# Optimization experiments

Measured on AMD Instinct MI355X. Metric: run time of the kernel, lower is better.

## Reference

```python
import jax, jax.numpy as jnp
import numpy as np
from jax import lax


def _sobel_kernels3d(n1=1, n2=2, n3=2):
    Sx = np.asarray([[[-n1, 0, n1], [-n2, 0, n2], [-n1, 0, n1]],
                     [[-n2, 0, n2], [-n3 * n2, 0, n3 * n2], [-n2, 0, n2]],
                     [[-n1, 0, n1], [-n2, 0, n2], [-n1, 0, n1]]])
    Sy = np.asarray([[[-n1, -n2, -n1], [0, 0, 0], [n1, n2, n1]],
                     [[-n2, -n3 * n2, -n2], [0, 0, 0], [n2, n3 * n2, n2]],
                     [[-n1, -n2, -n1], [0, 0, 0], [n1, n2, n1]]])
    Sz = np.asarray([[[-n1, -n2, -n1], [-n2, -n3 * n2, -n2], [-n1, -n2, -n1]],
                     [[0, 0, 0], [0, 0, 0], [0, 0, 0]],
                     [[n1, n2, n1], [n2, n3 * n2, n2], [n1, n2, n1]]])
    Sd11 = np.asarray([[[0, n1, n2], [-n1, 0, n1], [-n2, -n1, 0]],
                       [[0, n2, n2 * n3], [-n2, 0, n2], [-n2 * n3, -n2, 0]],
                       [[0, n1, n2], [-n1, 0, n1], [-n2, -n1, 0]]])
    Sd12 = np.asarray([[[-n2, -n1, 0], [-n1, 0, n1], [0, n1, n2]],
                       [[-n2 * n3, -n2, 0], [-n2, 0, n2], [0, n2, n2 * n3]],
                       [[-n2, -n1, 0], [-n1, 0, n1], [0, n1, n2]]])
    Sd21 = Sd11.T
    Sd22 = Sd12.T
    Sd31 = np.asarray([-S.T for S in Sd11.T])
    Sd32 = np.asarray([S.T for S in Sd12.T])
    S = [Sx, Sy, Sz, Sd11, Sd12, Sd21, Sd22, Sd31, Sd32]
    # (9, 1, 3, 3, 3) OIDHW conv weight bank
    return np.stack(S).astype(np.float32)[:, None]


def _grad_edge3d(img, kernels, a=1):
    # img: (B, C, H, W, D); kernels: (9, 1, 3, 3, 3)
    B, C, H, W, D = img.shape
    p = jnp.pad(img, ((0, 0), (0, 0), (a, a), (a, a), (a, a)), mode='reflect')
    Hp, Wp, Dp = H + 2 * a, W + 2 * a, D + 2 * a
    # Each channel convolved independently with all 9 kernels in one conv call.
    xin = p.reshape(B * C, 1, Hp, Wp, Dp)
    conv = lax.conv_general_dilated(
        xin, kernels, window_strides=(1, 1, 1), padding='SAME',
        dimension_numbers=('NCDHW', 'OIDHW', 'NCDHW'))  # (B*C, 9, Hp, Wp, Dp)
    conv = conv.reshape(B, C, 9, Hp, Wp, Dp)
    # torch: sum_c (conv + 1e-6), squared per-filter, then sum_s (. + 1e-6), sqrt, * 1/C
    per_filter = jnp.sum(conv + 1e-6, axis=1)           # (B, 9, Hp, Wp, Dp)
    mag = jnp.sqrt(jnp.sum(per_filter ** 2, axis=1) + 9 * 1e-6) / C  # (B, Hp, Wp, Dp)
    mag = mag[:, a:-a, a:-a, a:-a]                      # (B, H, W, D)
    mn = mag.min()
    mx = mag.max()
    norm = (mag - mn) / (mx - mn + 1e-6)
    return norm.reshape(B, 1, H, W, D)


def setup_inputs() -> dict:
    key = jax.random.key(0)
    kx, ky = jax.random.split(key)
    B, C, H, W, D = 4, 1, 128, 128, 128
    x = jax.random.normal(kx, (B, C, H, W, D), dtype=jnp.float32)
    y = jax.random.normal(ky, (B, C, H, W, D), dtype=jnp.float32)
    kernels = jnp.asarray(_sobel_kernels3d(1, 2, 2))
    return {"x": x, "y": y, "kernels": kernels}


def reference(x, y, kernels):
    edge_x = _grad_edge3d(x, kernels)
    edge_y = _grad_edge3d(y, kernels)
    # lam_errors = [(1.0, L1Loss())], reduction='sum' -> 1e-6 + 1.0 * mean|ex-ey|
    l1 = jnp.mean(jnp.abs(edge_x - edge_y))
    return 1e-6 + 1.0 * l1
```

## Files before the change

### kernel.cpp

```cpp
#include <hip/hip_runtime.h>
#include <hip/hip_fp16.h>

#define HH 128
#define NB 4
#define NVOX (NB * HH * HH * HH)

#define NBLK1 1024
#define GRID2 512
#define TPB 256

typedef float vf2 __attribute__((ext_vector_type(2)));

__device__ __align__(16) unsigned int g_bmin[NBLK1];
__device__ __align__(16) unsigned int g_bmax[NBLK1];

union U4H8 { uint4 u; __half2 h[4]; };

__global__ __launch_bounds__(256) void pass1_kernel(
    const float* __restrict__ x, const float* __restrict__ y,
    __half* __restrict__ magx, __half* __restrict__ magy,
    float* __restrict__ out) {
    int bid = blockIdx.x;
    int tid = threadIdx.x;
    if (bid == 0 && tid == 0) out[0] = 0.0f;

    int lane = tid & 63, wid = tid >> 6;
    int wg  = bid & 15;
    int hs  = (bid >> 4) & 7;
    int b   = (bid >> 7) & 3;
    int img = bid >> 9;

    const float* __restrict__ src = img ? y : x;
    __half* __restrict__ dst = img ? magy : magx;

    int w0 = wg * 8 + wid * 2;
    int w1 = w0 + 1;
    int cw0 = (w0 == 0) ? 1 : (w0 - 1);
    int cw3 = (w1 == 127) ? 126 : (w1 + 1);
    int h0 = hs << 4;
    const vf2* base2 = (const vf2*)(src + ((size_t)b << 21));

    const vf2 two = {2.0f, 2.0f};
    const vf2 e1v = {1e-6f, 1e-6f};

    vf2 sbD[2][3], ubD[2][3], dbS[2][3], sbS[2][3], ubS[2][3], dbU[2][3], sbU[2][3];
    float mn = 3.4e38f, mx = 0.0f;
    bool l0 = (lane == 0), l63 = (lane == 63);

    auto cstage = [&](vf2 q, vf2& S, vf2& D, vf2& U) {
        float Lxs = __shfl_up(q.y, 1);
        float Rys = __shfl_down(q.x, 1);
        float Lx = l0  ? q.y : Lxs;
        float Ry = l63 ? q.x : Rys;
        vf2 LV = {Lx, q.x};
        vf2 RV = {q.y, Ry};
        vf2 t = LV + RV;
        S = __builtin_elementwise_fma(two, q, t);
        D = RV - LV;
        U = t + q;
    };

#pragma unroll
    for (int r = 0; r < 18; ++r) {
        int hr = h0 + r - 1;
        hr = (hr < 0) ? 1 : ((hr > 127) ? 126 : hr);
        int rowb = (hr << 7);
        vf2 q0 = base2[(size_t)((rowb + cw0) << 6) + lane];
        vf2 q1 = base2[(size_t)((rowb + w0)  << 6) + lane];
        vf2 q2 = base2[(size_t)((rowb + w1)  << 6) + lane];
        vf2 q3 = base2[(size_t)((rowb + cw3) << 6) + lane];

        vf2 S[4], D[4], U[4];
        cstage(q0, S[0], D[0], U[0]);
        cstage(q1, S[1], D[1], U[1]);
        cstage(q2, S[2], D[2], U[2]);
        cstage(q3, S[3], D[3], U[3]);

        int slot = r % 3;
#pragma unroll
        for (int o = 0; o < 2; ++o) {
            vf2 D0 = D[o], D1 = D[o + 1], D2 = D[o + 2];
            vf2 S0 = S[o], S1 = S[o + 1], S2 = S[o + 2];
            vf2 U0 = U[o], U1 = U[o + 1], U2 = U[o + 2];
            vf2 tD = D0 + D2;
            sbD[o][slot] = __builtin_elementwise_fma(two, D1, tD);
            ubD[o][slot] = tD + D1;
            vf2 tS = S0 + S2;
            sbS[o][slot] = __builtin_elementwise_fma(two, S1, tS);
            ubS[o][slot] = tS + S1;
            dbS[o][slot] = S2 - S0;
            vf2 tU = U0 + U2;
            sbU[o][slot] = __builtin_elementwise_fma(two, U1, tU);
            dbU[o][slot] = U2 - U0;
        }

        if (r >= 2) {
            int s0 = (r - 2) % 3, s1 = (r - 1) % 3, s2 = slot;
            int hout = h0 + r - 2;
#pragma unroll
            for (int o = 0; o < 2; ++o) {
                vf2 tsbD = sbD[o][s0] + sbD[o][s2];
                vf2 Gssd = __builtin_elementwise_fma(two, sbD[o][s1], tsbD);
                vf2 Gusd = tsbD + sbD[o][s1];
                vf2 tubD = ubD[o][s0] + ubD[o][s2];
                vf2 Gsud = __builtin_elementwise_fma(two, ubD[o][s1], tubD);
                vf2 tdbS = dbS[o][s0] + dbS[o][s2];
                vf2 Gsds = __builtin_elementwise_fma(two, dbS[o][s1], tdbS);
                vf2 Guds = tdbS + dbS[o][s1];
                vf2 Gdss = sbS[o][s2] - sbS[o][s0];
                vf2 Gdus = ubS[o][s2] - ubS[o][s0];
                vf2 tdbU = dbU[o][s0] + dbU[o][s2];
                vf2 Gsdu = __builtin_elementwise_fma(two, dbU[o][s1], tdbU);
                vf2 Gdsu = sbU[o][s2] - sbU[o][s0];

                vf2 f0 = Gssd;
                vf2 f1 = Gsds;
                vf2 f2 = Gdss;
                vf2 f3 = Gsud - Gsdu;
                vf2 f4 = Gsud + Gsdu;
                vf2 f5 = Gdus - Guds;
                vf2 f6 = Gdus + Guds;
                vf2 f7 = Gusd - Gdsu;
                vf2 f8 = Gusd + Gdsu;

                vf2 s = {9.0f * 1e-6f, 9.0f * 1e-6f};
                vf2 u;
                u = f0 + e1v; s = __builtin_elementwise_fma(u, u, s);
                u = f1 + e1v; s = __builtin_elementwise_fma(u, u, s);
                u = f2 + e1v; s = __builtin_elementwise_fma(u, u, s);
                u = f3 + e1v; s = __builtin_elementwise_fma(u, u, s);
                u = f4 + e1v; s = __builtin_elementwise_fma(u, u, s);
                u = f5 + e1v; s = __builtin_elementwise_fma(u, u, s);
                u = f6 + e1v; s = __builtin_elementwise_fma(u, u, s);
                u = f7 + e1v; s = __builtin_elementwise_fma(u, u, s);
                u = f8 + e1v; s = __builtin_elementwise_fma(u, u, s);

                float2 m2;
                m2.x = sqrtf(s.x);
                m2.y = sqrtf(s.y);

                __half2 hm2 = __float22half2_rn(m2);
                float2 mr = __half22float2(hm2);
                int h2idx = (((b * 128 + hout) * 128 + (w0 + o)) << 6) + lane;
                __builtin_nontemporal_store(*(unsigned int*)&hm2,
                    (unsigned int*)((__half2*)dst + h2idx));
                mn = fminf(mn, fminf(mr.x, mr.y));
                mx = fmaxf(mx, fmaxf(mr.x, mr.y));
            }
        }
    }

    unsigned int umn = __float_as_uint(mn);
    unsigned int umx = __float_as_uint(mx);
#pragma unroll
    for (int off = 32; off > 0; off >>= 1) {
        unsigned int a1 = __shfl_down(umn, off, 64);
        unsigned int b1 = __shfl_down(umx, off, 64);
        umn = (a1 < umn) ? a1 : umn;
        umx = (b1 > umx) ? b1 : umx;
    }
    __shared__ unsigned int smn[4], smx[4];
    if (lane == 0) { smn[wid] = umn; smx[wid] = umx; }
    __syncthreads();
    if (tid == 0) {
        unsigned int m0 = smn[0] < smn[1] ? smn[0] : smn[1];
        unsigned int m1 = smn[2] < smn[3] ? smn[2] : smn[3];
        unsigned int x0 = smx[0] > smx[1] ? smx[0] : smx[1];
        unsigned int x1 = smx[2] > smx[3] ? smx[2] : smx[3];
        g_bmin[bid] = (m0 < m1 ? m0 : m1);
        g_bmax[bid] = (x0 > x1 ? x0 : x1);
    }
}

__global__ __launch_bounds__(TPB) void pass2_kernel(
    const uint4* __restrict__ magx8, const uint4* __restrict__ magy8,
    float* __restrict__ out) {
    int tid = threadIdx.x, bid = blockIdx.x;
    int lane = tid & 63, wid = tid >> 6;
    __shared__ unsigned int sred[4][4];
    __shared__ float smm[4];
    __shared__ float sv[4];

    const uint4* bmin4 = (const uint4*)g_bmin;
    const uint4* bmax4 = (const uint4*)g_bmax;
    unsigned int v0 = 0xFFFFFFFFu, v1 = 0u, v2 = 0xFFFFFFFFu, v3 = 0u;
    if (tid < 128) {
        uint4 a = bmin4[tid];
        uint4 b = bmax4[tid];
        uint4 c = bmin4[tid + 128];
        uint4 d = bmax4[tid + 128];
        unsigned int a01 = (a.x < a.y) ? a.x : a.y, a23 = (a.z < a.w) ? a.z : a.w;
        unsigned int b01 = (b.x > b.y) ? b.x : b.y, b23 = (b.z > b.w) ? b.z : b.w;
        unsigned int c01 = (c.x < c.y) ? c.x : c.y, c23 = (c.z < c.w) ? c.z : c.w;
        unsigned int d01 = (d.x > d.y) ? d.x : d.y, d23 = (d.z > d.w) ? d.z : d.w;
        v0 = (a01 < a23) ? a01 : a23;
        v1 = (b01 > b23) ? b01 : b23;
        v2 = (c01 < c23) ? c01 : c23;
        v3 = (d01 > d23) ? d01 : d23;
    }
#pragma unroll
    for (int off = 32; off > 0; off >>= 1) {
        unsigned int t0 = __shfl_down(v0, off, 64);
        unsigned int t1 = __shfl_down(v1, off, 64);
        unsigned int t2 = __shfl_down(v2, off, 64);
        unsigned int t3 = __shfl_down(v3, off, 64);
        v0 = (t0 < v0) ? t0 : v0;
        v1 = (t1 > v1) ? t1 : v1;
        v2 = (t2 < v2) ? t2 : v2;
        v3 = (t3 > v3) ? t3 : v3;
    }
    if (lane == 0) { sred[wid][0] = v0; sred[wid][1] = v1; sred[wid][2] = v2; sred[wid][3] = v3; }
    __syncthreads();
    if (tid == 0) {
        unsigned int r0 = sred[0][0], r1 = sred[0][1], r2 = sred[0][2], r3 = sred[0][3];
#pragma unroll
        for (int w = 1; w < 4; ++w) {
            r0 = (sred[w][0] < r0) ? sred[w][0] : r0;
            r1 = (sred[w][1] > r1) ? sred[w][1] : r1;
            r2 = (sred[w][2] < r2) ? sred[w][2] : r2;
            r3 = (sred[w][3] > r3) ? sred[w][3] : r3;
        }
        smm[0] = __uint_as_float(r0);
        smm[1] = __uint_as_float(r1);
        smm[2] = __uint_as_float(r2);
        smm[3] = __uint_as_float(r3);
    }
    __syncthreads();

    float mnx = smm[0], mxx = smm[1], mny = smm[2], mxy = smm[3];
    float ix = 1.0f / (mxx - mnx + 1e-6f);
    float iy = 1.0f / (mxy - mny + 1e-6f);
    float cx = -mnx * ix;
    float cy = -mny * iy;

    float s = 0.0f;
#pragma unroll
    for (int k = 0; k < 8; ++k) {
        int i = bid * 2048 + k * TPB + tid;
        U4H8 qa, qb;
        qa.u = magx8[i];
        qb.u = magy8[i];
#pragma unroll
        for (int j = 0; j < 4; ++j) {
            float2 va = __half22float2(qa.h[j]);
            float2 vb = __half22float2(qb.h[j]);
            s += fabsf(fmaf(va.x, ix, cx) - fmaf(vb.x, iy, cy));
            s += fabsf(fmaf(va.y, ix, cx) - fmaf(vb.y, iy, cy));
        }
    }
#pragma unroll
    for (int off = 32; off > 0; off >>= 1) s += __shfl_down(s, off, 64);
    if (lane == 0) sv[wid] = s;
    __syncthreads();
    if (tid == 0) {
        float partial = ((sv[0] + sv[1]) + (sv[2] + sv[3])) * (1.0f / (float)NVOX);
        if (bid == 0) partial += 1e-6f;
        atomicAdd(out, partial);
    }
}

extern "C" void kernel_launch(void* const* d_in, const int* in_sizes, int n_in,
                              void* d_out, int out_size, void* d_ws, size_t ws_size,
                              hipStream_t stream) {
    const float* x = (const float*)d_in[0];
    const float* y = (const float*)d_in[1];
    float* out = (float*)d_out;

    __half* magx = (__half*)d_ws;
    __half* magy = magx + NVOX;

    pass1_kernel<<<NBLK1, 256, 0, stream>>>(x, y, magx, magy, out);
    pass2_kernel<<<GRID2, TPB, 0, stream>>>((const uint4*)magx, (const uint4*)magy, out);
}
```

Baseline: 131.7 us.

## Halve h-slab per block, merge filter-pair squares, defer sqrt in min/max

Doubles the pass-1 grid by giving each block 8 output rows instead of 16, which raises parallelism but increases the fraction of redundant halo row loads. Adds an occupancy hint to launch bounds. Replaces the nine explicit filter squares with an algebraic identity ((a-b)^2+(a+b)^2 = 2a^2+2b^2), so the diagonal pairs need fewer operations. Tracks min/max on the squared sum and applies sqrt and half rounding only once per block. Pass 2 is adapted to read 2048 block partials.

After: 340.8 us. 159% more time.

```diff
diff --git a/kernel.cpp b/kernel.cpp
--- a/kernel.cpp
+++ b/kernel.cpp
@@ -5,7 +5,7 @@
 #define NB 4
 #define NVOX (NB * HH * HH * HH)
 
-#define NBLK1 1024
+#define NBLK1 2048
 #define GRID2 512
 #define TPB 256
 
@@ -16,7 +16,7 @@
 
 union U4H8 { uint4 u; __half2 h[4]; };
 
-__global__ __launch_bounds__(256) void pass1_kernel(
+__global__ __launch_bounds__(256, 8) void pass1_kernel(
     const float* __restrict__ x, const float* __restrict__ y,
     __half* __restrict__ magx, __half* __restrict__ magy,
     float* __restrict__ out) {
@@ -26,9 +26,9 @@
 
     int lane = tid & 63, wid = tid >> 6;
     int wg  = bid & 15;
-    int hs  = (bid >> 4) & 7;
-    int b   = (bid >> 7) & 3;
-    int img = bid >> 9;
+    int hs  = (bid >> 4) & 15;
+    int b   = (bid >> 8) & 3;
+    int img = bid >> 10;
 
     const float* __restrict__ src = img ? y : x;
     __half* __restrict__ dst = img ? magy : magx;
@@ -37,14 +37,15 @@
     int w1 = w0 + 1;
     int cw0 = (w0 == 0) ? 1 : (w0 - 1);
     int cw3 = (w1 == 127) ? 126 : (w1 + 1);
-    int h0 = hs << 4;
+    int h0 = hs << 3;
     const vf2* base2 = (const vf2*)(src + ((size_t)b << 21));
 
     const vf2 two = {2.0f, 2.0f};
     const vf2 e1v = {1e-6f, 1e-6f};
 
     vf2 sbD[2][3], ubD[2][3], dbS[2][3], sbS[2][3], ubS[2][3], dbU[2][3], sbU[2][3];
-    float mn = 3.4e38f, mx = 0.0f;
+    vf2 smn = {3.4e38f, 3.4e38f};
+    vf2 smx = {0.0f, 0.0f};
     bool l0 = (lane == 0), l63 = (lane == 63);
 
     auto cstage = [&](vf2 q, vf2& S, vf2& D, vf2& U) {
@@ -61,7 +62,7 @@
     };
 
 #pragma unroll
-    for (int r = 0; r < 18; ++r) {
+    for (int r = 0; r < 10; ++r) {
         int hr = h0 + r - 1;
         hr = (hr < 0) ? 1 : ((hr > 127) ? 126 : hr);
         int rowb = (hr << 7);
@@ -113,45 +114,35 @@
                 vf2 Gsdu = __builtin_elementwise_fma(two, dbU[o][s1], tdbU);
                 vf2 Gdsu = sbU[o][s2] - sbU[o][s0];
 
-                vf2 f0 = Gssd;
-                vf2 f1 = Gsds;
-                vf2 f2 = Gdss;
-                vf2 f3 = Gsud - Gsdu;
-                vf2 f4 = Gsud + Gsdu;
-                vf2 f5 = Gdus - Guds;
-                vf2 f6 = Gdus + Guds;
-                vf2 f7 = Gusd - Gdsu;
-                vf2 f8 = Gusd + Gdsu;
-
-                vf2 s = {9.0f * 1e-6f, 9.0f * 1e-6f};
+                vf2 s1v = {9.0f * 1e-6f, 9.0f * 1e-6f};
                 vf2 u;
-                u = f0 + e1v; s = __builtin_elementwise_fma(u, u, s);
-                u = f1 + e1v; s = __builtin_elementwise_fma(u, u, s);
-                u = f2 + e1v; s = __builtin_elementwise_fma(u, u, s);
-                u = f3 + e1v; s = __builtin_elementwise_fma(u, u, s);
-                u = f4 + e1v; s = __builtin_elementwise_fma(u, u, s);
-                u = f5 + e1v; s = __builtin_elementwise_fma(u, u, s);
-                u = f6 + e1v; s = __builtin_elementwise_fma(u, u, s);
-                u = f7 + e1v; s = __builtin_elementwise_fma(u, u, s);
-                u = f8 + e1v; s = __builtin_elementwise_fma(u, u, s);
+                u = Gssd + e1v; s1v = __builtin_elementwise_fma(u, u, s1v);
+                u = Gsds + e1v; s1v = __builtin_elementwise_fma(u, u, s1v);
+                u = Gdss + e1v; s1v = __builtin_elementwise_fma(u, u, s1v);
+                u = Gsud + e1v; vf2 s2v = u * u;
+                s2v = __builtin_elementwise_fma(Gsdu, Gsdu, s2v);
+                u = Gdus + e1v; s2v = __builtin_elementwise_fma(u, u, s2v);
+                s2v = __builtin_elementwise_fma(Guds, Guds, s2v);
+                u = Gusd + e1v; s2v = __builtin_elementwise_fma(u, u, s2v);
+                s2v = __builtin_elementwise_fma(Gdsu, Gdsu, s2v);
+                vf2 s = __builtin_elementwise_fma(two, s2v, s1v);
+
+                smn = __builtin_elementwise_min(smn, s);
+                smx = __builtin_elementwise_max(smx, s);
 
                 float2 m2;
                 m2.x = sqrtf(s.x);
                 m2.y = sqrtf(s.y);
-
                 __half2 hm2 = __float22half2_rn(m2);
-                float2 mr = __half22float2(hm2);
                 int h2idx = (((b * 128 + hout) * 128 + (w0 + o)) << 6) + lane;
                 __builtin_nontemporal_store(*(unsigned int*)&hm2,
                     (unsigned int*)((__half2*)dst + h2idx));
-                mn = fminf(mn, fminf(mr.x, mr.y));
-                mx = fmaxf(mx, fmaxf(mr.x, mr.y));
             }
         }
     }
 
-    unsigned int umn = __float_as_uint(mn);
-    unsigned int umx = __float_as_uint(mx);
+    unsigned int umn = __float_as_uint(fminf(smn.x, smn.y));
+    unsigned int umx = __float_as_uint(fmaxf(smx.x, smx.y));
 #pragma unroll
     for (int off = 32; off > 0; off >>= 1) {
         unsigned int a1 = __shfl_down(umn, off, 64);
@@ -159,16 +150,20 @@
         umn = (a1 < umn) ? a1 : umn;
         umx = (b1 > umx) ? b1 : umx;
     }
-    __shared__ unsigned int smn[4], smx[4];
-    if (lane == 0) { smn[wid] = umn; smx[wid] = umx; }
+    __shared__ unsigned int smnsh[4], smxsh[4];
+    if (lane == 0) { smnsh[wid] = umn; smxsh[wid] = umx; }
     __syncthreads();
     if (tid == 0) {
-        unsigned int m0 = smn[0] < smn[1] ? smn[0] : smn[1];
-        unsigned int m1 = smn[2] < smn[3] ? smn[2] : smn[3];
-        unsigned int x0 = smx[0] > smx[1] ? smx[0] : smx[1];
-        unsigned int x1 = smx[2] > smx[3] ? smx[2] : smx[3];
-        g_bmin[bid] = (m0 < m1 ? m0 : m1);
-        g_bmax[bid] = (x0 > x1 ? x0 : x1);
+        unsigned int m0 = smnsh[0] < smnsh[1] ? smnsh[0] : smnsh[1];
+        unsigned int m1 = smnsh[2] < smnsh[3] ? smnsh[2] : smnsh[3];
+        unsigned int x0 = smxsh[0] > smxsh[1] ? smxsh[0] : smxsh[1];
+        unsigned int x1 = smxsh[2] > smxsh[3] ? smxsh[2] : smxsh[3];
+        float ms = __uint_as_float(m0 < m1 ? m0 : m1);
+        float xs = __uint_as_float(x0 > x1 ? x0 : x1);
+        float mnm = __half2float(__float2half_rn(sqrtf(ms)));
+        float mxm = __half2float(__float2half_rn(sqrtf(xs)));
+        g_bmin[bid] = __float_as_uint(mnm);
+        g_bmax[bid] = __float_as_uint(mxm);
     }
 }
 
@@ -183,21 +178,18 @@
 
     const uint4* bmin4 = (const uint4*)g_bmin;
     const uint4* bmax4 = (const uint4*)g_bmax;
-    unsigned int v0 = 0xFFFFFFFFu, v1 = 0u, v2 = 0xFFFFFFFFu, v3 = 0u;
-    if (tid < 128) {
-        uint4 a = bmin4[tid];
-        uint4 b = bmax4[tid];
-        uint4 c = bmin4[tid + 128];
-        uint4 d = bmax4[tid + 128];
-        unsigned int a01 = (a.x < a.y) ? a.x : a.y, a23 = (a.z < a.w) ? a.z : a.w;
-        unsigned int b01 = (b.x > b.y) ? b.x : b.y, b23 = (b.z > b.w) ? b.z : b.w;
-        unsigned int c01 = (c.x < c.y) ? c.x : c.y, c23 = (c.z < c.w) ? c.z : c.w;
-        unsigned int d01 = (d.x > d.y) ? d.x : d.y, d23 = (d.z > d.w) ? d.z : d.w;
-        v0 = (a01 < a23) ? a01 : a23;
-        v1 = (b01 > b23) ? b01 : b23;
-        v2 = (c01 < c23) ? c01 : c23;
-        v3 = (d01 > d23) ? d01 : d23;
-    }
+    uint4 a = bmin4[tid];
+    uint4 bq = bmax4[tid];
+    uint4 c = bmin4[tid + 256];
+    uint4 d = bmax4[tid + 256];
+    unsigned int a01 = (a.x < a.y) ? a.x : a.y, a23 = (a.z < a.w) ? a.z : a.w;
+    unsigned int b01 = (bq.x > bq.y) ? bq.x : bq.y, b23 = (bq.z > bq.w) ? bq.z : bq.w;
+    unsigned int c01 = (c.x < c.y) ? c.x : c.y, c23 = (c.z < c.w) ? c.z : c.w;
+    unsigned int d01 = (d.x > d.y) ? d.x : d.y, d23 = (d.z > d.w) ? d.z : d.w;
+    unsigned int v0 = (a01 < a23) ? a01 : a23;
+    unsigned int v1 = (b01 > b23) ? b01 : b23;
+    unsigned int v2 = (c01 < c23) ? c01 : c23;
+    unsigned int v3 = (d01 > d23) ? d01 : d23;
 #pragma unroll
     for (int off = 32; off > 0; off >>= 1) {
         unsigned int t0 = __shfl_down(v0, off, 64);
```
